# Kernel tuning notes

Hardware: AMD Instinct MI355X
Metric: run time of the kernel (lower is better)

The kernel has to match this reference:

```python
import jax, jax.numpy as jnp
import numpy as np

N = 30000   # num_nodes
E = 480000  # num_edges (avg degree 16)
R = 8       # num_relations
B = 4       # num_bases
H = 128     # h_dim
OUT = 128   # out_dim


def setup_inputs() -> dict:
    key = jax.random.key(0)
    ks = jax.random.split(key, 16)
    s = 0.05
    return {
        "x": jnp.arange(N, dtype=jnp.int32),
        "src": jax.random.randint(ks[0], (E,), 0, N, dtype=jnp.int32),
        "dst": jax.random.randint(ks[1], (E,), 0, N, dtype=jnp.int32),
        "rel": jax.random.randint(ks[2], (E,), 0, R, dtype=jnp.int32),
        "norm": jax.random.uniform(ks[3], (E,), dtype=jnp.float32),
        # input layer (featureless: in_feat == num_nodes, basis decomposition)
        "V_in": jax.random.normal(ks[4], (B, N, H), dtype=jnp.float32) * s,
        "comp_in": jax.random.normal(ks[5], (R, B), dtype=jnp.float32) * 0.5,
        "bias_in": jnp.zeros((H,), dtype=jnp.float32),
        # hidden layer
        "V_h": jax.random.normal(ks[6], (B, H, H), dtype=jnp.float32) * s,
        "comp_h": jax.random.normal(ks[7], (R, B), dtype=jnp.float32) * 0.5,
        "bias_h": jnp.zeros((H,), dtype=jnp.float32),
        # output layer
        "V_out": jax.random.normal(ks[8], (B, H, OUT), dtype=jnp.float32) * s,
        "comp_out": jax.random.normal(ks[9], (R, B), dtype=jnp.float32) * 0.5,
        "bias_out": jnp.zeros((OUT,), dtype=jnp.float32),
        # GlobalAttentionPooling gate_nn: Linear(out_dim, 1)
        "gate_W": jax.random.normal(ks[10], (OUT, 1), dtype=jnp.float32) * s,
        "gate_b": jnp.zeros((1,), dtype=jnp.float32),
    }


def _rgc_dense(h, src, dst, rel, norm, V, comp, bias):
    """RelGraphConv (basis) for dense node features h: [N, in]."""
    c = comp[rel]          # [E, B] per-edge basis coefficients
    hs = h[src]            # [E, in] gather source features
    m = jnp.zeros((hs.shape[0], V.shape[-1]), dtype=h.dtype)
    for b in range(V.shape[0]):  # small fixed loop over bases
        m = m + c[:, b:b + 1] * (hs @ V[b])
    m = m * norm[:, None]
    return jax.ops.segment_sum(m, dst, num_segments=N) + bias


def _rgc_idfeat(x, src, dst, rel, norm, V, comp, bias):
    """Input RelGraphConv with node-ID features (one-hot == row gather)."""
    Wfull = jnp.einsum('rb,bno->rno', comp, V)    # [R, N, H]
    m = Wfull[rel, x[src]] * norm[:, None]        # [E, H]
    return jax.ops.segment_sum(m, dst, num_segments=N) + bias


def reference(x, src, dst, rel, norm,
              V_in, comp_in, bias_in,
              V_h, comp_h, bias_h,
              V_out, comp_out, bias_out,
              gate_W, gate_b):
    h = _rgc_idfeat(x, src, dst, rel, norm, V_in, comp_in, bias_in)
    h = jax.nn.relu(h)  # dropout p=0.0 -> identity
    h = _rgc_dense(h, src, dst, rel, norm, V_h, comp_h, bias_h)
    h = jax.nn.relu(h)
    h = _rgc_dense(h, src, dst, rel, norm, V_out, comp_out, bias_out)
    # GlobalAttentionPooling (single graph): softmax over nodes
    gate = jax.nn.softmax(h @ gate_W + gate_b, axis=0)  # [N, 1]
    return jnp.sum(gate * h, axis=0)  # [OUT]
```

## Files before the change

### kernel.cpp

```cpp
#include <hip/hip_runtime.h>
#include <hip/hip_bf16.h>

#define NN 30000
#define EE 480000
#define RR 8
#define BB 4
#define HH 128
#define NH (NN * HH)
#define NCAP 30016
#define CH 8
#define CSLOT 16
#define NN64 (NN * 64)

typedef __attribute__((ext_vector_type(8))) short short8;
typedef __attribute__((ext_vector_type(4))) float float4v;

__device__ __forceinline__ unsigned short f2bf(float f) {
    union { float f; unsigned int i; } c; c.f = f;
    unsigned int r = c.i + 0x7fffu + ((c.i >> 16) & 1u);
    return (unsigned short)(r >> 16);
}
__device__ __forceinline__ float bflo(unsigned int v) {
    union { unsigned int i; float f; } c; c.i = v << 16; return c.f;
}
__device__ __forceinline__ float bfhi(unsigned int v) {
    union { unsigned int i; float f; } c; c.i = v & 0xFFFF0000u; return c.f;
}
__device__ __forceinline__ unsigned int packbf(float a, float b) {
    return (unsigned int)f2bf(a) | ((unsigned int)f2bf(b) << 16);
}

#define SCAT_BLOCKS 469
#define TBL_BLOCKS 1875
#define BTF_BLOCKS 512
__global__ __launch_bounds__(256)
void k_mix(const int* __restrict__ dst, const int* __restrict__ src,
           const int* __restrict__ rel, const float* __restrict__ norm,
           int* __restrict__ cnt, unsigned int* __restrict__ meta,
           const float* __restrict__ V_in, const float* __restrict__ comp_in,
           unsigned int* __restrict__ table_u,
           const float* __restrict__ V_h, const float* __restrict__ V_o,
           unsigned short* __restrict__ Btf_h, unsigned short* __restrict__ Btf_o,
           float* __restrict__ scal, float* __restrict__ out) {
    int bid = blockIdx.x;
    if (bid < SCAT_BLOCKS) {
        int c = bid & 7;
        int base = bid * 1024 + threadIdx.x;
        int d[4]; unsigned int u[4]; bool ok[4];
#pragma unroll
        for (int e = 0; e < 4; ++e) {
            int i = base + e * 256;
            ok[e] = i < EE;
            d[e] = ok[e] ? dst[i] : 0;
            int sv = ok[e] ? src[i] : 0;
            int rv = ok[e] ? rel[i] : 0;
            float nv = ok[e] ? norm[i] : 0.f;
            unsigned int nq = (unsigned int)(nv * 16383.f + 0.5f);
            u[e] = (nq << 18) | ((unsigned int)rv << 15) | (unsigned int)sv;
        }
        int p[4];
#pragma unroll
        for (int e = 0; e < 4; ++e)
            if (ok[e]) p[e] = atomicAdd(&cnt[c * NCAP + d[e]], 1);
#pragma unroll
        for (int e = 0; e < 4; ++e)
            if (ok[e] && p[e] < CSLOT)
                meta[(c * NCAP + d[e]) * CSLOT + p[e]] = u[e];
    } else if (bid < SCAT_BLOCKS + TBL_BLOCKS) {
        int idx = ((bid - SCAT_BLOCKS) * 256 + threadIdx.x) * 8;
        float4v va[4], vb[4];
#pragma unroll
        for (int b = 0; b < 4; ++b) {
            va[b] = *(const float4v*)(V_in + b * NH + idx);
            vb[b] = *(const float4v*)(V_in + b * NH + idx + 4);
        }
#pragma unroll
        for (int r = 0; r < RR; ++r) {
            float c0 = comp_in[r * 4 + 0], c1 = comp_in[r * 4 + 1];
            float c2 = comp_in[r * 4 + 2], c3 = comp_in[r * 4 + 3];
            float4v oa = c0 * va[0] + c1 * va[1] + c2 * va[2] + c3 * va[3];
            float4v ob = c0 * vb[0] + c1 * vb[1] + c2 * vb[2] + c3 * vb[3];
            uint4 sv;
            sv.x = packbf(oa[0], oa[1]); sv.y = packbf(oa[2], oa[3]);
            sv.z = packbf(ob[0], ob[1]); sv.w = packbf(ob[2], ob[3]);
            *(uint4*)(table_u + (r * NH + idx) / 2) = sv;
        }
    } else {
        if (bid == SCAT_BLOCKS + TBL_BLOCKS) {
            if (threadIdx.x == 0) scal[0] = 0.f;
            if (threadIdx.x >= 128) out[threadIdx.x - 128] = 0.f;
        }
        int idx = (bid - SCAT_BLOCKS - TBL_BLOCKS) * 256 + threadIdx.x;
        int which = idx >> 16;
        int local = idx & 0xFFFF;
        int j = local >> 9;
        int k = local & 511;
        const float* V = which ? V_o : V_h;
        unsigned short* W = which ? Btf_o : Btf_h;
        int half = k >> 8, kk = (k >> 5) & 7, kq = (k >> 3) & 3, e = k & 7;
        int c = j >> 4, mr = j & 15;
        int fi = half * 32768 + ((((kk * 4 + kq) * 8 + c) * 16 + mr) * 8 + e);
        W[fi] = f2bf(V[k * 128 + j]);
    }
}

__global__ __launch_bounds__(256)
void k_agg1(const unsigned int* __restrict__ table_u, const int* __restrict__ cnt,
            const unsigned int* __restrict__ meta, const float* __restrict__ bias,
            unsigned int* __restrict__ h1u) {
    __shared__ int s_row[4][128];
    __shared__ float s_wt[4][128];
    int tid = threadIdx.x;
    int w = tid >> 6, lane = tid & 63;
    int d = blockIdx.x * 4 + w;
    int s = lane & 15, cg = lane >> 4;
    int cn0 = cnt[cg * NCAP + d]; if (cn0 > CSLOT) cn0 = CSLOT;
    int cn1 = cnt[(cg + 4) * NCAP + d]; if (cn1 > CSLOT) cn1 = CSLOT;
    bool v0 = s < cn0, v1 = s < cn1;
    unsigned int m0 = v0 ? meta[(cg * NCAP + d) * CSLOT + s] : 0u;
    unsigned int m1 = v1 ? meta[((cg + 4) * NCAP + d) * CSLOT + s] : 0u;
    unsigned long long bal0 = __ballot(v0);
    unsigned long long bal1 = __ballot(v1);
    unsigned long long below = (1ULL << lane) - 1ULL;
    int tot0 = __popcll(bal0);
    if (v0) {
        int idx = __popcll(bal0 & below);
        s_row[w][idx] = (int)(((m0 >> 15) & 7u) * (unsigned int)NN64 + (m0 & 0x7FFFu) * 64u);
        s_wt[w][idx] = (float)(m0 >> 18) * (1.f / 16383.f);
    }
    if (v1) {
        int idx = tot0 + __popcll(bal1 & below);
        s_row[w][idx] = (int)(((m1 >> 15) & 7u) * (unsigned int)NN64 + (m1 & 0x7FFFu) * 64u);
        s_wt[w][idx] = (float)(m1 >> 18) * (1.f / 16383.f);
    }
    int cn = tot0 + __popcll(bal1);
    __syncthreads();
    float a0 = 0.f, a1 = 0.f, b0 = 0.f, b1 = 0.f;
    int j = 0;
    for (; j + 8 <= cn; j += 8) {
        int r[8]; float wt[8]; unsigned int v[8];
#pragma unroll
        for (int e = 0; e < 8; ++e) { r[e] = s_row[w][j + e]; wt[e] = s_wt[w][j + e]; }
#pragma unroll
        for (int e = 0; e < 8; ++e) v[e] = table_u[r[e] + lane];
#pragma unroll
        for (int e = 0; e < 8; ++e) {
            if (e & 1) { b0 += wt[e] * bflo(v[e]); b1 += wt[e] * bfhi(v[e]); }
            else       { a0 += wt[e] * bflo(v[e]); a1 += wt[e] * bfhi(v[e]); }
        }
    }
    for (; j + 4 <= cn; j += 4) {
        int r[4]; float wt[4]; unsigned int v[4];
#pragma unroll
        for (int e = 0; e < 4; ++e) { r[e] = s_row[w][j + e]; wt[e] = s_wt[w][j + e]; }
#pragma unroll
        for (int e = 0; e < 4; ++e) v[e] = table_u[r[e] + lane];
#pragma unroll
        for (int e = 0; e < 4; ++e) {
            if (e & 1) { b0 += wt[e] * bflo(v[e]); b1 += wt[e] * bfhi(v[e]); }
            else       { a0 += wt[e] * bflo(v[e]); a1 += wt[e] * bfhi(v[e]); }
        }
    }
    for (; j < cn; ++j) {
        int r0 = s_row[w][j];
        float w0 = s_wt[w][j];
        unsigned int v0 = table_u[r0 + lane];
        a0 += w0 * bflo(v0); a1 += w0 * bfhi(v0);
    }
    a0 += b0 + bias[2 * lane];
    a1 += b1 + bias[2 * lane + 1];
    a0 = fmaxf(a0, 0.f); a1 = fmaxf(a1, 0.f);
    h1u[d * 64 + lane] = packbf(a0, a1);
}

#define FT_ROWS 32
#define FT_BLOCKS (NCAP / FT_ROWS)
__global__ __launch_bounds__(512)
void k_fused(const unsigned int* __restrict__ hu, const int* __restrict__ cnt,
             const unsigned int* __restrict__ meta, const float* __restrict__ comp,
             const unsigned short* __restrict__ Btf, const float* __restrict__ bias,
             unsigned int* __restrict__ outu, int relu,
             const float* __restrict__ gW, const float* __restrict__ gb,
             float* __restrict__ wexp, float* __restrict__ scal) {
    __shared__ __align__(16) unsigned short Asm[FT_ROWS * 512];
    __shared__ unsigned int s_meta[8][128];
    __shared__ float4v s_comp4[8];
    __shared__ float s_ls[8];
    int tid = threadIdx.x;
    int w = tid >> 6, lane = tid & 63;
    if (tid < 32) ((float*)s_comp4)[tid] = comp[tid];
    __syncthreads();
    int m0 = blockIdx.x * FT_ROWS;
    int s = lane & 15, cg = lane >> 4;
    unsigned long long below = (1ULL << lane) - 1ULL;
    for (int t = 0; t < 4; ++t) {
        int d = m0 + w * 4 + t;
        int cn0 = cnt[cg * NCAP + d]; if (cn0 > CSLOT) cn0 = CSLOT;
        int cn1 = cnt[(cg + 4) * NCAP + d]; if (cn1 > CSLOT) cn1 = CSLOT;
        bool v0 = s < cn0, v1 = s < cn1;
        unsigned int mm0 = v0 ? meta[(cg * NCAP + d) * CSLOT + s] : 0u;
        unsigned int mm1 = v1 ? meta[((cg + 4) * NCAP + d) * CSLOT + s] : 0u;
        unsigned long long bal0 = __ballot(v0);
        unsigned long long bal1 = __ballot(v1);
        int tot0 = __popcll(bal0);
        if (v0) s_meta[w][__popcll(bal0 & below)] = mm0;
        if (v1) s_meta[w][tot0 + __popcll(bal1 & below)] = mm1;
        int cn = tot0 + __popcll(bal1);
        float a00 = 0, a01 = 0, a10 = 0, a11 = 0, a20 = 0, a21 = 0, a30 = 0, a31 = 0;
        int j = 0;
        for (; j + 8 <= cn; j += 8) {
            unsigned int mm[8]; unsigned int v[8];
#pragma unroll
            for (int e = 0; e < 8; ++e) mm[e] = s_meta[w][j + e];
#pragma unroll
            for (int e = 0; e < 8; ++e) v[e] = hu[((mm[e] & 0x7FFFu) << 6) + lane];
#pragma unroll
            for (int e = 0; e < 8; ++e) {
                float4v wv = s_comp4[(mm[e] >> 15) & 7u];
                float nm = (float)(mm[e] >> 18) * (1.f / 16383.f);
                float w0 = wv[0] * nm, w1 = wv[1] * nm;
                float w2 = wv[2] * nm, w3 = wv[3] * nm;
                float f0 = bflo(v[e]), f1 = bfhi(v[e]);
                a00 += w0 * f0; a01 += w0 * f1;
                a10 += w1 * f0; a11 += w1 * f1;
                a20 += w2 * f0; a21 += w2 * f1;
                a30 += w3 * f0; a31 += w3 * f1;
            }
        }
        for (; j < cn; ++j) {
            unsigned int mm = s_meta[w][j];
            unsigned int v = hu[((mm & 0x7FFFu) << 6) + lane];
            float4v wv = s_comp4[(mm >> 15) & 7u];
            float nm = (float)(mm >> 18) * (1.f / 16383.f);
            float w0 = wv[0] * nm, w1 = wv[1] * nm;
            float w2 = wv[2] * nm, w3 = wv[3] * nm;
            float f0 = bflo(v), f1 = bfhi(v);
            a00 += w0 * f0; a01 += w0 * f1;
            a10 += w1 * f0; a11 += w1 * f1;
            a20 += w2 * f0; a21 += w2 * f1;
            a30 += w3 * f0; a31 += w3 * f1;
        }
        int row = w * 4 + t;
        char* base = (char*)Asm + row * 1024;
        unsigned int sw = (unsigned int)((row & 7) << 4);
        *(unsigned int*)(base + ((0u * 256u + lane * 4u) ^ sw)) = packbf(a00, a01);
        *(unsigned int*)(base + ((1u * 256u + lane * 4u) ^ sw)) = packbf(a10, a11);
        *(unsigned int*)(base + ((2u * 256u + lane * 4u) ^ sw)) = packbf(a20, a21);
        *(unsigned int*)(base + ((3u * 256u + lane * 4u) ^ sw)) = packbf(a30, a31);
    }
    __syncthreads();
    int mr = lane & 15, kq = lane >> 4;
    int rw = w & 1, cb = w >> 1;
    int arow = rw * 16 + mr;
    const char* abase = (const char*)Asm + arow * 1024;
    unsigned int swr = (unsigned int)((arow & 7) << 4);
    float4v z = {0.f, 0.f, 0.f, 0.f};
    float4v acc0 = z, acc1 = z;
#pragma unroll
    for (int half = 0; half < 2; ++half) {
#pragma unroll
        for (int kk = 0; kk < 8; ++kk) {
            short8 a = *(const short8*)(abase +
                        ((unsigned int)(half * 512 + kk * 64 + kq * 16) ^ swr));
            int c0 = cb * 2;
            short8 bv0 = *(const short8*)(Btf + half * 32768 +
                          ((((kk * 4 + kq) * 8 + c0) * 16 + mr) << 3));
            short8 bv1 = *(const short8*)(Btf + half * 32768 +
                          ((((kk * 4 + kq) * 8 + c0 + 1) * 16 + mr) << 3));
            acc0 = __builtin_amdgcn_mfma_f32_16x16x32_bf16(a, bv0, acc0, 0, 0, 0);
            acc1 = __builtin_amdgcn_mfma_f32_16x16x32_bf16(a, bv1, acc1, 0, 0, 0);
        }
    }
    __syncthreads();
    float* lds = (float*)Asm;
#pragma unroll
    for (int i = 0; i < 4; ++i) {
        lds[(rw * 16 + kq * 4 + i) * 132 + (cb * 2) * 16 + mr] = acc0[i];
        lds[(rw * 16 + kq * 4 + i) * 132 + (cb * 2 + 1) * 16 + mr] = acc1[i];
    }
    __syncthreads();
    float b0 = bias[2 * lane], b1 = bias[2 * lane + 1];
    float gw0 = 0.f, gw1 = 0.f, gb0 = 0.f, lsum = 0.f;
    if (wexp) { gw0 = gW[2 * lane]; gw1 = gW[2 * lane + 1]; gb0 = gb[0]; }
    for (int it = 0; it < 4; ++it) {
        int node = m0 + w * 4 + it;
        if (node < NN) {
            float f0 = lds[(w * 4 + it) * 132 + 2 * lane] + b0;
            float f1 = lds[(w * 4 + it) * 132 + 2 * lane + 1] + b1;
            if (relu) { f0 = fmaxf(f0, 0.f); f1 = fmaxf(f1, 0.f); }
            if (wexp) {
                float p = f0 * gw0 + f1 * gw1;
#pragma unroll
                for (int off = 32; off; off >>= 1) p += __shfl_down(p, off);
                if (lane == 0) {
                    float we = __expf(p + gb0);
                    wexp[node] = we;
                    lsum += we;
                }
            }
            outu[node * 64 + lane] = packbf(f0, f1);
        }
    }
    if (wexp) {
        if (lane == 0) s_ls[w] = lsum;
        __syncthreads();
        if (tid == 0) {
            float t = s_ls[0] + s_ls[1] + s_ls[2] + s_ls[3]
                    + s_ls[4] + s_ls[5] + s_ls[6] + s_ls[7];
            atomicAdd(&scal[0], t);
        }
    }
}

__global__ __launch_bounds__(256)
void k_out(const unsigned int* __restrict__ h3u, const float* __restrict__ wexp,
           const float* __restrict__ scal, float* __restrict__ out) {
    __shared__ float s_acc[4][128];
    int tid = threadIdx.x;
    int w = tid >> 6, h = tid & 63;
    int n0 = blockIdx.x * 256 + w * 64;
    int n1 = n0 + 64; if (n1 > NN) n1 = NN;
    float inv = 1.f / scal[0];
    float a0 = 0.f, a1 = 0.f, b0 = 0.f, b1 = 0.f;
    int n = n0;
    for (; n + 2 <= n1; n += 2) {
        float wa = wexp[n] * inv;
        float wb = wexp[n + 1] * inv;
        unsigned int va = h3u[n * 64 + h];
        unsigned int vb = h3u[(n + 1) * 64 + h];
        a0 += wa * bflo(va); a1 += wa * bfhi(va);
        b0 += wb * bflo(vb); b1 += wb * bfhi(vb);
    }
    for (; n < n1; ++n) {
        float wa = wexp[n] * inv;
        unsigned int va = h3u[n * 64 + h];
        a0 += wa * bflo(va); a1 += wa * bfhi(va);
    }
    s_acc[w][2 * h] = a0 + b0;
    s_acc[w][2 * h + 1] = a1 + b1;
    __syncthreads();
    if (tid < 128) {
        float t = s_acc[0][tid] + s_acc[1][tid] + s_acc[2][tid] + s_acc[3][tid];
        atomicAdd(&out[tid], t);
    }
}

extern "C" void kernel_launch(void* const* d_in, const int* in_sizes, int n_in,
                              void* d_out, int out_size, void* d_ws, size_t ws_size,
                              hipStream_t stream) {
    const int* src = (const int*)d_in[1];
    const int* dst = (const int*)d_in[2];
    const int* rel = (const int*)d_in[3];
    const float* norm = (const float*)d_in[4];
    const float* V_in = (const float*)d_in[5];
    const float* comp_in = (const float*)d_in[6];
    const float* bias_in = (const float*)d_in[7];
    const float* V_h = (const float*)d_in[8];
    const float* comp_h = (const float*)d_in[9];
    const float* bias_h = (const float*)d_in[10];
    const float* V_out = (const float*)d_in[11];
    const float* comp_out = (const float*)d_in[12];
    const float* bias_out = (const float*)d_in[13];
    const float* gate_W = (const float*)d_in[14];
    const float* gate_b = (const float*)d_in[15];
    float* out = (float*)d_out;

    char* ws = (char*)d_ws;
    unsigned short* table = (unsigned short*)ws;
    unsigned int* h1u = (unsigned int*)(ws + 61440000);
    unsigned int* h2u = (unsigned int*)(ws + 69120000);
    unsigned int* h3u = (unsigned int*)(ws + 76800000);
    unsigned short* Btf_h = (unsigned short*)(ws + 84480000);
    unsigned short* Btf_o = (unsigned short*)(ws + 84611072);
    int* cnt = (int*)(ws + 84742144);
    unsigned int* meta = (unsigned int*)(ws + 85702656);
    float* wexp = (float*)(ws + 101070848);
    float* scal = (float*)(ws + 101190848);

    hipMemsetAsync(cnt, 0, CH * NCAP * sizeof(int), stream);
    k_mix<<<SCAT_BLOCKS + TBL_BLOCKS + BTF_BLOCKS, 256, 0, stream>>>(
        dst, src, rel, norm, cnt, meta, V_in, comp_in, (unsigned int*)table,
        V_h, V_out, Btf_h, Btf_o, scal, out);

    k_agg1<<<NN / 4, 256, 0, stream>>>((const unsigned int*)table, cnt, meta, bias_in, h1u);

    k_fused<<<FT_BLOCKS, 512, 0, stream>>>(h1u, cnt, meta, comp_h, Btf_h, bias_h, h2u, 1,
                                           (const float*)nullptr, (const float*)nullptr,
                                           (float*)nullptr, (float*)nullptr);

    k_fused<<<FT_BLOCKS, 512, 0, stream>>>(h2u, cnt, meta, comp_out, Btf_o, bias_out, h3u, 0,
                                           gate_W, gate_b, wexp, scal);

    k_out<<<(NN + 255) / 256, 256, 0, stream>>>(h3u, wexp, scal, out);
}
```

Measured before the change: 283.7 us.

## Interleave two destination nodes per wave in gather loops and shrink fused tiles

The edge-gather loops in k_agg1 and k_fused now process two destination nodes per wavefront at once, issuing 16 independent row loads per iteration instead of 8. The goal is more memory-level parallelism to hide gather latency. k_fused also moves from 32-row, 512-thread blocks to 16-row, 256-thread blocks, with the MFMA tile mapping rewritten so each wave covers two column blocks of one 16-row tile. The cost is higher register pressure from the doubled accumulators and loaded values, and remainder loops that run serially once the two nodes' edge counts diverge.

```diff
diff --git a/kernel.cpp b/kernel.cpp
--- a/kernel.cpp
+++ b/kernel.cpp
@@ -104,78 +104,149 @@
     }
 }
 
+__device__ __forceinline__ void agg1_fin(const unsigned int* __restrict__ table_u,
+        const int* sr, const float* swt, int lane, int j, int cn,
+        float& a0, float& a1, float& b0, float& b1) {
+    for (; j + 8 <= cn; j += 8) {
+        int r[8]; float wt[8]; unsigned int v[8];
+#pragma unroll
+        for (int e = 0; e < 8; ++e) { r[e] = sr[j + e]; wt[e] = swt[j + e]; }
+#pragma unroll
+        for (int e = 0; e < 8; ++e) v[e] = table_u[r[e] + lane];
+#pragma unroll
+        for (int e = 0; e < 8; ++e) {
+            if (e & 1) { b0 += wt[e] * bflo(v[e]); b1 += wt[e] * bfhi(v[e]); }
+            else       { a0 += wt[e] * bflo(v[e]); a1 += wt[e] * bfhi(v[e]); }
+        }
+    }
+    for (; j + 4 <= cn; j += 4) {
+        int r[4]; float wt[4]; unsigned int v[4];
+#pragma unroll
+        for (int e = 0; e < 4; ++e) { r[e] = sr[j + e]; wt[e] = swt[j + e]; }
+#pragma unroll
+        for (int e = 0; e < 4; ++e) v[e] = table_u[r[e] + lane];
+#pragma unroll
+        for (int e = 0; e < 4; ++e) {
+            if (e & 1) { b0 += wt[e] * bflo(v[e]); b1 += wt[e] * bfhi(v[e]); }
+            else       { a0 += wt[e] * bflo(v[e]); a1 += wt[e] * bfhi(v[e]); }
+        }
+    }
+    for (; j < cn; ++j) {
+        int r0 = sr[j];
+        float w0 = swt[j];
+        unsigned int v0 = table_u[r0 + lane];
+        a0 += w0 * bflo(v0); a1 += w0 * bfhi(v0);
+    }
+}
+
 __global__ __launch_bounds__(256)
 void k_agg1(const unsigned int* __restrict__ table_u, const int* __restrict__ cnt,
             const unsigned int* __restrict__ meta, const float* __restrict__ bias,
             unsigned int* __restrict__ h1u) {
-    __shared__ int s_row[4][128];
-    __shared__ float s_wt[4][128];
+    __shared__ int s_row[4][2][128];
+    __shared__ float s_wt[4][2][128];
     int tid = threadIdx.x;
     int w = tid >> 6, lane = tid & 63;
-    int d = blockIdx.x * 4 + w;
+    int dbase = blockIdx.x * 8 + w * 2;
     int s = lane & 15, cg = lane >> 4;
-    int cn0 = cnt[cg * NCAP + d]; if (cn0 > CSLOT) cn0 = CSLOT;
-    int cn1 = cnt[(cg + 4) * NCAP + d]; if (cn1 > CSLOT) cn1 = CSLOT;
-    bool v0 = s < cn0, v1 = s < cn1;
-    unsigned int m0 = v0 ? meta[(cg * NCAP + d) * CSLOT + s] : 0u;
-    unsigned int m1 = v1 ? meta[((cg + 4) * NCAP + d) * CSLOT + s] : 0u;
-    unsigned long long bal0 = __ballot(v0);
-    unsigned long long bal1 = __ballot(v1);
     unsigned long long below = (1ULL << lane) - 1ULL;
-    int tot0 = __popcll(bal0);
-    if (v0) {
-        int idx = __popcll(bal0 & below);
-        s_row[w][idx] = (int)(((m0 >> 15) & 7u) * (unsigned int)NN64 + (m0 & 0x7FFFu) * 64u);
-        s_wt[w][idx] = (float)(m0 >> 18) * (1.f / 16383.f);
-    }
-    if (v1) {
-        int idx = tot0 + __popcll(bal1 & below);
-        s_row[w][idx] = (int)(((m1 >> 15) & 7u) * (unsigned int)NN64 + (m1 & 0x7FFFu) * 64u);
-        s_wt[w][idx] = (float)(m1 >> 18) * (1.f / 16383.f);
-    }
-    int cn = tot0 + __popcll(bal1);
-    __syncthreads();
-    float a0 = 0.f, a1 = 0.f, b0 = 0.f, b1 = 0.f;
-    int j = 0;
+    int cnv[2];
+#pragma unroll
+    for (int rr = 0; rr < 2; ++rr) {
+        int d = dbase + rr;
+        int cn0 = cnt[cg * NCAP + d]; if (cn0 > CSLOT) cn0 = CSLOT;
+        int cn1 = cnt[(cg + 4) * NCAP + d]; if (cn1 > CSLOT) cn1 = CSLOT;
+        bool v0 = s < cn0, v1 = s < cn1;
+        unsigned int m0 = v0 ? meta[(cg * NCAP + d) * CSLOT + s] : 0u;
+        unsigned int m1 = v1 ? meta[((cg + 4) * NCAP + d) * CSLOT + s] : 0u;
+        unsigned long long bal0 = __ballot(v0);
+        unsigned long long bal1 = __ballot(v1);
+        int tot0 = __popcll(bal0);
+        if (v0) {
+            int idx = __popcll(bal0 & below);
+            s_row[w][rr][idx] = (int)(((m0 >> 15) & 7u) * (unsigned int)NN64 + (m0 & 0x7FFFu) * 64u);
+            s_wt[w][rr][idx] = (float)(m0 >> 18) * (1.f / 16383.f);
+        }
+        if (v1) {
+            int idx = tot0 + __popcll(bal1 & below);
+            s_row[w][rr][idx] = (int)(((m1 >> 15) & 7u) * (unsigned int)NN64 + (m1 & 0x7FFFu) * 64u);
+            s_wt[w][rr][idx] = (float)(m1 >> 18) * (1.f / 16383.f);
+        }
+        cnv[rr] = tot0 + __popcll(bal1);
+    }
+    float aA0 = 0, aA1 = 0, bA0 = 0, bA1 = 0;
+    float aB0 = 0, aB1 = 0, bB0 = 0, bB1 = 0;
+    int jA = 0, jB = 0;
+    while (jA + 8 <= cnv[0] && jB + 8 <= cnv[1]) {
+        int rA[8], rB[8]; float wA[8], wB[8]; unsigned int vA[8], vB[8];
+#pragma unroll
+        for (int e = 0; e < 8; ++e) { rA[e] = s_row[w][0][jA + e]; wA[e] = s_wt[w][0][jA + e]; }
+#pragma unroll
+        for (int e = 0; e < 8; ++e) { rB[e] = s_row[w][1][jB + e]; wB[e] = s_wt[w][1][jB + e]; }
+#pragma unroll
+        for (int e = 0; e < 8; ++e) vA[e] = table_u[rA[e] + lane];
+#pragma unroll
+        for (int e = 0; e < 8; ++e) vB[e] = table_u[rB[e] + lane];
+#pragma unroll
+        for (int e = 0; e < 8; ++e) {
+            if (e & 1) { bA0 += wA[e] * bflo(vA[e]); bA1 += wA[e] * bfhi(vA[e]); }
+            else       { aA0 += wA[e] * bflo(vA[e]); aA1 += wA[e] * bfhi(vA[e]); }
+        }
+#pragma unroll
+        for (int e = 0; e < 8; ++e) {
+            if (e & 1) { bB0 += wB[e] * bflo(vB[e]); bB1 += wB[e] * bfhi(vB[e]); }
+            else       { aB0 += wB[e] * bflo(vB[e]); aB1 += wB[e] * bfhi(vB[e]); }
+        }
+        jA += 8; jB += 8;
+    }
+    agg1_fin(table_u, s_row[w][0], s_wt[w][0], lane, jA, cnv[0], aA0, aA1, bA0, bA1);
+    agg1_fin(table_u, s_row[w][1], s_wt[w][1], lane, jB, cnv[1], aB0, aB1, bB0, bB1);
+    float bias0 = bias[2 * lane], bias1 = bias[2 * lane + 1];
+    aA0 += bA0 + bias0; aA1 += bA1 + bias1;
+    aA0 = fmaxf(aA0, 0.f); aA1 = fmaxf(aA1, 0.f);
+    h1u[dbase * 64 + lane] = packbf(aA0, aA1);
+    aB0 += bB0 + bias0; aB1 += bB1 + bias1;
+    aB0 = fmaxf(aB0, 0.f); aB1 = fmaxf(aB1, 0.f);
+    h1u[(dbase + 1) * 64 + lane] = packbf(aB0, aB1);
+}
+
+#define FT_ROWS 16
+#define FT_BLOCKS (NCAP / FT_ROWS)
+struct Acc8 { float a00, a01, a10, a11, a20, a21, a30, a31; };
+
+__device__ __forceinline__ void fma_edge(Acc8& A, unsigned int mm, unsigned int v,
+                                         const float4v* s_comp4) {
+    float4v wv = s_comp4[(mm >> 15) & 7u];
+    float nm = (float)(mm >> 18) * (1.f / 16383.f);
+    float w0 = wv[0] * nm, w1 = wv[1] * nm;
+    float w2 = wv[2] * nm, w3 = wv[3] * nm;
+    float f0 = bflo(v), f1 = bfhi(v);
+    A.a00 += w0 * f0; A.a01 += w0 * f1;
+    A.a10 += w1 * f0; A.a11 += w1 * f1;
+    A.a20 += w2 * f0; A.a21 += w2 * f1;
+    A.a30 += w3 * f0; A.a31 += w3 * f1;
+}
+
+__device__ __forceinline__ void fused_fin(const unsigned int* __restrict__ hu,
+        const unsigned int* sm, int j, int cn, int lane,
+        const float4v* s_comp4, Acc8& A) {
     for (; j + 8 <= cn; j += 8) {
-        int r[8]; float wt[8]; unsigned int v[8];
-#pragma unroll
-        for (int e = 0; e < 8; ++e) { r[e] = s_row[w][j + e]; wt[e] = s_wt[w][j + e]; }
-#pragma unroll
-        for (int e = 0; e < 8; ++e) v[e] = table_u[r[e] + lane];
-#pragma unroll
-        for (int e = 0; e < 8; ++e) {
-            if (e & 1) { b0 += wt[e] * bflo(v[e]); b1 += wt[e] * bfhi(v[e]); }
-            else       { a0 += wt[e] * bflo(v[e]); a1 += wt[e] * bfhi(v[e]); }
-        }
-    }
-    for (; j + 4 <= cn; j += 4) {
-        int r[4]; float wt[4]; unsigned int v[4];
-#pragma unroll
-        for (int e = 0; e < 4; ++e) { r[e] = s_row[w][j + e]; wt[e] = s_wt[w][j + e]; }
-#pragma unroll
-        for (int e = 0; e < 4; ++e) v[e] = table_u[r[e] + lane];
-#pragma unroll
-        for (int e = 0; e < 4; ++e) {
-            if (e & 1) { b0 += wt[e] * bflo(v[e]); b1 += wt[e] * bfhi(v[e]); }
-            else       { a0 += wt[e] * bflo(v[e]); a1 += wt[e] * bfhi(v[e]); }
-        }
+        unsigned int mm[8], v[8];
+#pragma unroll
+        for (int e = 0; e < 8; ++e) mm[e] = sm[j + e];
+#pragma unroll
+        for (int e = 0; e < 8; ++e) v[e] = hu[((mm[e] & 0x7FFFu) << 6) + lane];
+#pragma unroll
+        for (int e = 0; e < 8; ++e) fma_edge(A, mm[e], v[e], s_comp4);
     }
     for (; j < cn; ++j) {
-        int r0 = s_row[w][j];
-        float w0 = s_wt[w][j];
-        unsigned int v0 = table_u[r0 + lane];
-        a0 += w0 * bflo(v0); a1 += w0 * bfhi(v0);
-    }
-    a0 += b0 + bias[2 * lane];
-    a1 += b1 + bias[2 * lane + 1];
-    a0 = fmaxf(a0, 0.f); a1 = fmaxf(a1, 0.f);
-    h1u[d * 64 + lane] = packbf(a0, a1);
-}
-
-#define FT_ROWS 32
-#define FT_BLOCKS (NCAP / FT_ROWS)
-__global__ __launch_bounds__(512)
+        unsigned int mm = sm[j];
+        unsigned int v = hu[((mm & 0x7FFFu) << 6) + lane];
+        fma_edge(A, mm, v, s_comp4);
+    }
+}
+
+__global__ __launch_bounds__(256)
 void k_fused(const unsigned int* __restrict__ hu, const int* __restrict__ cnt,
              const unsigned int* __restrict__ meta, const float* __restrict__ comp,
              const unsigned short* __restrict__ Btf, const float* __restrict__ bias,
@@ -183,9 +254,9 @@
              const float* __restrict__ gW, const float* __restrict__ gb,
              float* __restrict__ wexp, float* __restrict__ scal) {
     __shared__ __align__(16) unsigned short Asm[FT_ROWS * 512];
-    __shared__ unsigned int s_meta[8][128];
+    __shared__ unsigned int s_meta[4][2][128];
     __shared__ float4v s_comp4[8];
-    __shared__ float s_ls[8];
+    __shared__ float s_ls[4];
     int tid = threadIdx.x;
     int w = tid >> 6, lane = tid & 63;
     if (tid < 32) ((float*)s_comp4)[tid] = comp[tid];
@@ -193,76 +264,69 @@
     int m0 = blockIdx.x * FT_ROWS;
     int s = lane & 15, cg = lane >> 4;
     unsigned long long below = (1ULL << lane) - 1ULL;
-    for (int t = 0; t < 4; ++t) {
-        int d = m0 + w * 4 + t;
-        int cn0 = cnt[cg * NCAP + d]; if (cn0 > CSLOT) cn0 = CSLOT;
-        int cn1 = cnt[(cg + 4) * NCAP + d]; if (cn1 > CSLOT) cn1 = CSLOT;
-        bool v0 = s < cn0, v1 = s < cn1;
-        unsigned int mm0 = v0 ? meta[(cg * NCAP + d) * CSLOT + s] : 0u;
-        unsigned int mm1 = v1 ? meta[((cg + 4) * NCAP + d) * CSLOT + s] : 0u;
-        unsigned long long bal0 = __ballot(v0);
-        unsigned long long bal1 = __ballot(v1);
-        int tot0 = __popcll(bal0);
-        if (v0) s_meta[w][__popcll(bal0 & below)] = mm0;
-        if (v1) s_meta[w][tot0 + __popcll(bal1 & below)] = mm1;
-        int cn = tot0 + __popcll(bal1);
-        float a00 = 0, a01 = 0, a10 = 0, a11 = 0, a20 = 0, a21 = 0, a30 = 0, a31 = 0;
-        int j = 0;
-        for (; j + 8 <= cn; j += 8) {
-            unsigned int mm[8]; unsigned int v[8];
-#pragma unroll
-            for (int e = 0; e < 8; ++e) mm[e] = s_meta[w][j + e];
-#pragma unroll
-            for (int e = 0; e < 8; ++e) v[e] = hu[((mm[e] & 0x7FFFu) << 6) + lane];
-#pragma unroll
-            for (int e = 0; e < 8; ++e) {
-                float4v wv = s_comp4[(mm[e] >> 15) & 7u];
-                float nm = (float)(mm[e] >> 18) * (1.f / 16383.f);
-                float w0 = wv[0] * nm, w1 = wv[1] * nm;
-                float w2 = wv[2] * nm, w3 = wv[3] * nm;
-                float f0 = bflo(v[e]), f1 = bfhi(v[e]);
-                a00 += w0 * f0; a01 += w0 * f1;
-                a10 += w1 * f0; a11 += w1 * f1;
-                a20 += w2 * f0; a21 += w2 * f1;
-                a30 += w3 * f0; a31 += w3 * f1;
-            }
-        }
-        for (; j < cn; ++j) {
-            unsigned int mm = s_meta[w][j];
-            unsigned int v = hu[((mm & 0x7FFFu) << 6) + lane];
-            float4v wv = s_comp4[(mm >> 15) & 7u];
-            float nm = (float)(mm >> 18) * (1.f / 16383.f);
-            float w0 = wv[0] * nm, w1 = wv[1] * nm;
-            float w2 = wv[2] * nm, w3 = wv[3] * nm;
-            float f0 = bflo(v), f1 = bfhi(v);
-            a00 += w0 * f0; a01 += w0 * f1;
-            a10 += w1 * f0; a11 += w1 * f1;
-            a20 += w2 * f0; a21 += w2 * f1;
-            a30 += w3 * f0; a31 += w3 * f1;
-        }
-        int row = w * 4 + t;
-        char* base = (char*)Asm + row * 1024;
-        unsigned int sw = (unsigned int)((row & 7) << 4);
-        *(unsigned int*)(base + ((0u * 256u + lane * 4u) ^ sw)) = packbf(a00, a01);
-        *(unsigned int*)(base + ((1u * 256u + lane * 4u) ^ sw)) = packbf(a10, a11);
-        *(unsigned int*)(base + ((2u * 256u + lane * 4u) ^ sw)) = packbf(a20, a21);
-        *(unsigned int*)(base + ((3u * 256u + lane * 4u) ^ sw)) = packbf(a30, a31);
+#pragma unroll
+    for (int t2 = 0; t2 < 2; ++t2) {
+        int cnv[2];
+#pragma unroll
+        for (int rr = 0; rr < 2; ++rr) {
+            int d = m0 + w * 4 + t2 * 2 + rr;
+            int cn0 = cnt[cg * NCAP + d]; if (cn0 > CSLOT) cn0 = CSLOT;
+            int cn1 = cnt[(cg + 4) * NCAP + d]; if (cn1 > CSLOT) cn1 = CSLOT;
+            bool v0 = s < cn0, v1 = s < cn1;
+            unsigned int mm0 = v0 ? meta[(cg * NCAP + d) * CSLOT + s] : 0u;
+            unsigned int mm1 = v1 ? meta[((cg + 4) * NCAP + d) * CSLOT + s] : 0u;
+            unsigned long long bal0 = __ballot(v0);
+            unsigned long long bal1 = __ballot(v1);
+            int tot0 = __popcll(bal0);
+            if (v0) s_meta[w][rr][__popcll(bal0 & below)] = mm0;
+            if (v1) s_meta[w][rr][tot0 + __popcll(bal1 & below)] = mm1;
+            cnv[rr] = tot0 + __popcll(bal1);
+        }
+        Acc8 A = {}, B = {};
+        int jA = 0, jB = 0;
+        while (jA + 8 <= cnv[0] && jB + 8 <= cnv[1]) {
+            unsigned int mmA[8], mmB[8], vA[8], vB[8];
+#pragma unroll
+            for (int e = 0; e < 8; ++e) mmA[e] = s_meta[w][0][jA + e];
+#pragma unroll
+            for (int e = 0; e < 8; ++e) mmB[e] = s_meta[w][1][jB + e];
+#pragma unroll
+            for (int e = 0; e < 8; ++e) vA[e] = hu[((mmA[e] & 0x7FFFu) << 6) + lane];
+#pragma unroll
+            for (int e = 0; e < 8; ++e) vB[e] = hu[((mmB[e] & 0x7FFFu) << 6) + lane];
+#pragma unroll
+            for (int e = 0; e < 8; ++e) fma_edge(A, mmA[e], vA[e], s_comp4);
+#pragma unroll
+            for (int e = 0; e < 8; ++e) fma_edge(B, mmB[e], vB[e], s_comp4);
+            jA += 8; jB += 8;
+        }
+        fused_fin(hu, s_meta[w][0], jA, cnv[0], lane, s_comp4, A);
+        fused_fin(hu, s_meta[w][1], jB, cnv[1], lane, s_comp4, B);
+#pragma unroll
+        for (int rr = 0; rr < 2; ++rr) {
+            Acc8& X = rr ? B : A;
+            int row = w * 4 + t2 * 2 + rr;
+            char* base = (char*)Asm + row * 1024;
+            unsigned int sw = (unsigned int)((row & 7) << 4);
+            *(unsigned int*)(base + ((0u * 256u + lane * 4u) ^ sw)) = packbf(X.a00, X.a01);
+            *(unsigned int*)(base + ((1u * 256u + lane * 4u) ^ sw)) = packbf(X.a10, X.a11);
+            *(unsigned int*)(base + ((2u * 256u + lane * 4u) ^ sw)) = packbf(X.a20, X.a21);
+            *(unsigned int*)(base + ((3u * 256u + lane * 4u) ^ sw)) = packbf(X.a30, X.a31);
+        }
     }
     __syncthreads();
     int mr = lane & 15, kq = lane >> 4;
-    int rw = w & 1, cb = w >> 1;
-    int arow = rw * 16 + mr;
-    const char* abase = (const char*)Asm + arow * 1024;
-    unsigned int swr = (unsigned int)((arow & 7) << 4);
+    const char* abase = (const char*)Asm + mr * 1024;
+    unsigned int swr = (unsigned int)((mr & 7) << 4);
     float4v z = {0.f, 0.f, 0.f, 0.f};
     float4v acc0 = z, acc1 = z;
+    int c0 = w * 2;
 #pragma unroll
     for (int half = 0; half < 2; ++half) {
 #pragma unroll
         for (int kk = 0; kk < 8; ++kk) {
             short8 a = *(const short8*)(abase +
                         ((unsigned int)(half * 512 + kk * 64 + kq * 16) ^ swr));
-            int c0 = cb * 2;
             short8 bv0 = *(const short8*)(Btf + half * 32768 +
                           ((((kk * 4 + kq) * 8 + c0) * 16 + mr) << 3));
             short8 bv1 = *(const short8*)(Btf + half * 32768 +
@@ -275,18 +339,20 @@
     float* lds = (float*)Asm;
 #pragma unroll
     for (int i = 0; i < 4; ++i) {
-        lds[(rw * 16 + kq * 4 + i) * 132 + (cb * 2) * 16 + mr] = acc0[i];
-        lds[(rw * 16 + kq * 4 + i) * 132 + (cb * 2 + 1) * 16 + mr] = acc1[i];
+        lds[(kq * 4 + i) * 132 + c0 * 16 + mr] = acc0[i];
+        lds[(kq * 4 + i) * 132 + (c0 + 1) * 16 + mr] = acc1[i];
     }
     __syncthreads();
     float b0 = bias[2 * lane], b1 = bias[2 * lane + 1];
     float gw0 = 0.f, gw1 = 0.f, gb0 = 0.f, lsum = 0.f;
     if (wexp) { gw0 = gW[2 * lane]; gw1 = gW[2 * lane + 1]; gb0 = gb[0]; }
+#pragma unroll
     for (int it = 0; it < 4; ++it) {
-        int node = m0 + w * 4 + it;
+        int row = w * 4 + it;
+        int node = m0 + row;
         if (node < NN) {
-            float f0 = lds[(w * 4 + it) * 132 + 2 * lane] + b0;
-            float f1 = lds[(w * 4 + it) * 132 + 2 * lane + 1] + b1;
+            float f0 = lds[row * 132 + 2 * lane] + b0;
+            float f1 = lds[row * 132 + 2 * lane + 1] + b1;
             if (relu) { f0 = fmaxf(f0, 0.f); f1 = fmaxf(f1, 0.f); }
             if (wexp) {
                 float p = f0 * gw0 + f1 * gw1;
@@ -305,8 +371,7 @@
         if (lane == 0) s_ls[w] = lsum;
         __syncthreads();
         if (tid == 0) {
-            float t = s_ls[0] + s_ls[1] + s_ls[2] + s_ls[3]
-                    + s_ls[4] + s_ls[5] + s_ls[6] + s_ls[7];
+            float t = s_ls[0] + s_ls[1] + s_ls[2] + s_ls[3];
             atomicAdd(&scal[0], t);
         }
     }
@@ -382,13 +447,13 @@
         dst, src, rel, norm, cnt, meta, V_in, comp_in, (unsigned int*)table,
         V_h, V_out, Btf_h, Btf_o, scal, out);
 
-    k_agg1<<<NN / 4, 256, 0, stream>>>((const unsigned int*)table, cnt, meta, bias_in, h1u);
-
-    k_fused<<<FT_BLOCKS, 512, 0, stream>>>(h1u, cnt, meta, comp_h, Btf_h, bias_h, h2u, 1,
+    k_agg1<<<NN / 8, 256, 0, stream>>>((const unsigned int*)table, cnt, meta, bias_in, h1u);
+
+    k_fused<<<FT_BLOCKS, 256, 0, stream>>>(h1u, cnt, meta, comp_h, Btf_h, bias_h, h2u, 1,
                                            (const float*)nullptr, (const float*)nullptr,
                                            (float*)nullptr, (float*)nullptr);
 
-    k_fused<<<FT_BLOCKS, 512, 0, stream>>>(h2u, cnt, meta, comp_out, Btf_o, bias_out, h3u, 0,
+    k_fused<<<FT_BLOCKS, 256, 0, stream>>>(h2u, cnt, meta, comp_out, Btf_o, bias_out, h3u, 0,
                                            gate_W, gate_b, wexp, scal);
 
     k_out<<<(NN + 255) / 256, 256, 0, stream>>>(h3u, wexp, scal, out);
```

New measurement: 291.4 us. 2.7% more time.
